# Optimization experiments

Hardware: AMD Instinct MI355X
Metric: run time of the kernel (lower is better)

## Reference

```python
import jax, jax.numpy as jnp
import numpy as np

B, T, I, H = 32, 1024, 512, 512


def _uniform(key, shape, stdv):
    return jax.random.uniform(key, shape, jnp.float32, -stdv, stdv)


def setup_inputs() -> dict:
    key = jax.random.key(0)
    ks = jax.random.split(key, 13)
    stdv = 1.0 / np.sqrt(H)
    return {
        "z": jax.random.normal(ks[0], (B, T, I, 2), jnp.float32),
        "W_zi": _uniform(ks[1], (I, H, 2), stdv), "W_hi": _uniform(ks[2], (H, H, 2), stdv), "b_i": _uniform(ks[3], (H,), stdv),
        "W_zf": _uniform(ks[4], (I, H, 2), stdv), "W_hf": _uniform(ks[5], (H, H, 2), stdv), "b_f": _uniform(ks[6], (H,), stdv),
        "W_zc": _uniform(ks[7], (I, H, 2), stdv), "W_hc": _uniform(ks[8], (H, H, 2), stdv), "b_c": _uniform(ks[9], (H, 2), stdv),
        "W_zo": _uniform(ks[10], (I, H, 2), stdv), "W_ho": _uniform(ks[11], (H, H, 2), stdv), "b_o": _uniform(ks[12], (H,), stdv),
    }


def complex_tanh(zr, zi):
    mag = jnp.maximum(jnp.sqrt(zr * zr + zi * zi + 1e-14), 1e-8)
    t = jnp.tanh(mag)
    return t * (zr / mag), t * (zi / mag)


def reference(z, W_zi, W_hi, b_i, W_zf, W_hf, b_f, W_zc, W_hc, b_c, W_zo, W_ho, b_o):
    zr, zi = z[..., 0], z[..., 1]  # (B,T,I)

    def in_proj_real(Wz):  # real part of complex matmul z @ Wz
        return jnp.einsum('bti,ih->bth', zr, Wz[..., 0]) - jnp.einsum('bti,ih->bth', zi, Wz[..., 1])

    xi = in_proj_real(W_zi)
    xf = in_proj_real(W_zf)
    xo = in_proj_real(W_zo)
    xcr = in_proj_real(W_zc)
    xci = jnp.einsum('bti,ih->bth', zi, W_zc[..., 0]) + jnp.einsum('bti,ih->bth', zr, W_zc[..., 1])

    # time-major for scan: (T,B,H)
    xs = tuple(jnp.swapaxes(a, 0, 1) for a in (xi, xf, xo, xcr, xci))

    def step(carry, x):
        h_r, h_i, c_r, c_i = carry
        xi_t, xf_t, xo_t, xcr_t, xci_t = x
        i_t = jax.nn.sigmoid(xi_t + h_r @ W_hi[..., 0] - h_i @ W_hi[..., 1] + b_i)
        f_t = jax.nn.sigmoid(xf_t + h_r @ W_hf[..., 0] - h_i @ W_hf[..., 1] + b_f)
        o_t = jax.nn.sigmoid(xo_t + h_r @ W_ho[..., 0] - h_i @ W_ho[..., 1] + b_o)
        cr = xcr_t + h_r @ W_hc[..., 0] - h_i @ W_hc[..., 1] + b_c[..., 0]
        ci = xci_t + h_i @ W_hc[..., 0] + h_r @ W_hc[..., 1] + b_c[..., 1]
        ctr, cti = complex_tanh(cr, ci)
        c_r = f_t * c_r + i_t * ctr
        c_i = f_t * c_i + i_t * cti
        hr, hi = complex_tanh(c_r, c_i)
        h_r = o_t * hr
        h_i = o_t * hi
        return (h_r, h_i, c_r, c_i), jnp.stack((h_r, h_i), axis=-1)

    zero = jnp.zeros((z.shape[0], W_hi.shape[0]), z.dtype)
    (h_r, h_i, c_r, c_i), hs = jax.lax.scan(step, (zero, zero, zero, zero), xs)
    hidden_seq = jnp.swapaxes(hs, 0, 1)  # (B,T,H,2)
    h_t = jnp.stack((h_r, h_i), axis=-1)
    c_t = jnp.stack((c_r, c_i), axis=-1)
    return hidden_seq, (h_t, c_t)
```

## Files before the change

### kernel.cpp

```cpp
#include <hip/hip_runtime.h>


#define B_ 32
#define T_ 1024
#define Hd 512
#define Kd 1024
#define Nd 2560
#define Md 32768
#define HS_ELEMS 33554432ull

typedef __attribute__((ext_vector_type(8))) short bf16x8;
typedef __attribute__((ext_vector_type(4))) float f32x4;

__device__ __forceinline__ unsigned short f_bf(float f) {
  unsigned int x; __builtin_memcpy(&x, &f, 4);
  unsigned int r = (x + 0x7FFFu + ((x >> 16) & 1u)) >> 16;
  return (unsigned short)r;
}
__device__ __forceinline__ float bf_f(unsigned short u) {
  unsigned int i = ((unsigned int)u) << 16; float f; __builtin_memcpy(&f, &i, 4); return f;
}
__device__ __forceinline__ float fsig(float x) { return 1.0f / (1.0f + __expf(-x)); }
__device__ __forceinline__ void ctanh_(float zr, float zi, float& tr, float& ti) {
  float m2 = zr * zr + zi * zi + 1e-14f;
  float mag = __fsqrt_rn(m2);
  float e = __expf(2.0f * mag);
  float th = 1.0f - 2.0f / (e + 1.0f);
  float s = th / mag;
  tr = zr * s; ti = zi * s;
}

__device__ __forceinline__ void gl16(const unsigned short* g, unsigned short* l) {
  __builtin_amdgcn_global_load_lds(
      (const __attribute__((address_space(1))) void*)g,
      (__attribute__((address_space(3))) void*)l, 16, 0, 0);
}

__device__ __forceinline__ unsigned int ald(const unsigned int* p) {
  return __hip_atomic_load(p, __ATOMIC_RELAXED, __HIP_MEMORY_SCOPE_AGENT);
}
__device__ __forceinline__ void ast(unsigned int* p, unsigned int v) {
  __hip_atomic_store(p, v, __ATOMIC_RELAXED, __HIP_MEMORY_SCOPE_AGENT);
}

__global__ void build_weights(const float* Wzi, const float* Whi, const float* bi,
                              const float* Wzf, const float* Whf, const float* bfv,
                              const float* Wzc, const float* Whc, const float* bc,
                              const float* Wzo, const float* Who, const float* bo,
                              unsigned short* WzT, unsigned short* WhT, float* bcomb) {
  int n = blockIdx.x;
  int slab = n / 80, wi = n % 80, g = wi / 16, hh = slab * 16 + (wi & 15);
  const float *Wz, *Wh;
  if (g == 0)      { Wz = Wzi; Wh = Whi; }
  else if (g == 1) { Wz = Wzf; Wh = Whf; }
  else if (g == 2) { Wz = Wzo; Wh = Who; }
  else             { Wz = Wzc; Wh = Whc; }
  int q0, q1; float s0, s1;
  if (g < 4) { q0 = 0; s0 = 1.f; q1 = 1; s1 = -1.f; }
  else       { q0 = 1; s0 = 1.f; q1 = 0; s1 =  1.f; }
  for (int k = threadIdx.x; k < Kd; k += 256) {
    int j = k >> 1, p = k & 1;
    int q = p ? q1 : q0; float sg = p ? s1 : s0;
    WzT[(size_t)n * Kd + k] = f_bf(sg * Wz[(j * Hd + hh) * 2 + q]);
    WhT[(size_t)n * Kd + k] = f_bf(sg * Wh[(j * Hd + hh) * 2 + q]);
  }
  if (threadIdx.x == 0) {
    float bv;
    if (g == 0) bv = bi[hh]; else if (g == 1) bv = bfv[hh];
    else if (g == 2) bv = bo[hh];
    else if (g == 3) bv = bc[2 * hh]; else bv = bc[2 * hh + 1];
    bcomb[n] = bv;
  }
}

__global__ void cvt_z(const float4* __restrict__ z, ushort4* __restrict__ Z2) {
  for (size_t i = (size_t)blockIdx.x * 256 + threadIdx.x; i < 8388608ull; i += 8192ull * 256) {
    float4 v = z[i];
    ushort4 o;
    o.x = f_bf(v.x); o.y = f_bf(v.y); o.z = f_bf(v.z); o.w = f_bf(v.w);
    Z2[i] = o;
  }
}

__global__ __launch_bounds__(256) void gemm_x(const unsigned short* __restrict__ Z2,
                                              const unsigned short* __restrict__ WT,
                                              unsigned short* __restrict__ X) {
  __shared__ unsigned short As[128 * 64];
  __shared__ unsigned short Bs[128 * 64];
  int tid = threadIdx.x, lane = tid & 63, wv = tid >> 6;
  int bid = blockIdx.x;
  int mb = bid / (Nd / 128), nb = bid % (Nd / 128);
  size_t m0 = (size_t)mb * 128, n0 = (size_t)nb * 128;
  int wr = wv >> 1, wc = wv & 1;
  int l15 = lane & 15, kg = lane >> 4;
  int lrow = tid >> 3;
  int lcol = (tid & 7) * 8;
  f32x4 acc[4][4] = {};
  for (int k0 = 0; k0 < Kd; k0 += 64) {
    __syncthreads();
#pragma unroll
    for (int c = 0; c < 4; ++c) {
      gl16(Z2 + (m0 + c * 32 + lrow) * Kd + k0 + lcol,
           As + (size_t)c * 2048 + wv * 512);
      gl16(WT + (n0 + c * 32 + lrow) * Kd + k0 + lcol,
           Bs + (size_t)c * 2048 + wv * 512);
    }
    __syncthreads();
#pragma unroll
    for (int ks = 0; ks < 2; ++ks) {
      int kk = ks * 32 + kg * 8;
      bf16x8 a[4], b[4];
#pragma unroll
      for (int i = 0; i < 4; ++i)
        a[i] = *reinterpret_cast<const bf16x8*>(&As[(wr * 64 + i * 16 + l15) * 64 + kk]);
#pragma unroll
      for (int j = 0; j < 4; ++j)
        b[j] = *reinterpret_cast<const bf16x8*>(&Bs[(wc * 64 + j * 16 + l15) * 64 + kk]);
#pragma unroll
      for (int i = 0; i < 4; ++i)
#pragma unroll
        for (int j = 0; j < 4; ++j)
          acc[i][j] = __builtin_amdgcn_mfma_f32_16x16x32_bf16(a[i], b[j], acc[i][j], 0, 0, 0);
    }
  }
#pragma unroll
  for (int i = 0; i < 4; ++i)
#pragma unroll
    for (int j = 0; j < 4; ++j) {
      size_t gm = m0 + wr * 64 + i * 16 + kg * 4;
      size_t gn = n0 + wc * 64 + j * 16 + l15;
#pragma unroll
      for (int r = 0; r < 4; ++r)
        X[(gm + r) * Nd + gn] = f_bf(acc[i][j][r]);
    }
}

#define CHUNK 8
#define STEPB (Nd * 2)
__global__ __launch_bounds__(512) void lstm_all(
    const unsigned short* __restrict__ WhT, const unsigned short* __restrict__ X,
    const float* __restrict__ bcomb, unsigned short* __restrict__ hb,
    int* __restrict__ ctl, float* __restrict__ out) {
  __shared__ unsigned short Xs[2][CHUNK * STEPB / 2];
  __shared__ float xch[8][5][256];
  const int s = blockIdx.x;
  const int tid = threadIdx.x;
  const int wv = tid >> 6, lane = tid & 63;
  const int kh = wv >> 1, mh = wv & 1;
  const int l15 = lane & 15, kg = lane >> 4;
  const int cb = tid >> 4;
  const int ch = tid & 15;
  const int hh = s * 16 + ch;

  unsigned int* flags2 = (unsigned int*)(ctl + 16);
  unsigned int* hbu = (unsigned int*)hb;
  const int pidx = ((s >> 3) * 2 + (wv >> 2)) * 32 + (s & 7) * 4 + (wv & 3);
  const int fbase = (kh * 2 + mh) * 32;
  const int i32 = lane & 31;

  auto stage = [&](int tbase, int buf) {
#pragma unroll
    for (int j = 0; j < 5; ++j) {
      unsigned int P = (unsigned int)(wv * 5 + j) * 1024u + (unsigned int)lane * 16u;
      unsigned int st = P / STEPB, r = P % STEPB;
      unsigned int b = r / 160u, rem = r % 160u;
      gl16(X + ((size_t)b * T_ + (tbase + st)) * Nd + s * 80 + rem / 2,
           &Xs[buf][(size_t)(wv * 5 + j) * 512]);
    }
  };
  stage(0, 0);

  bf16x8 w[5][8];
#pragma unroll
  for (int g = 0; g < 5; ++g)
#pragma unroll
    for (int ks = 0; ks < 8; ++ks)
      w[g][ks] = *reinterpret_cast<const bf16x8*>(
          &WhT[(size_t)(s * 80 + g * 16 + l15) * Kd + kh * 256 + ks * 32 + kg * 8]);

  float bias[5];
#pragma unroll
  for (int g = 0; g < 5; ++g) bias[g] = bcomb[s * 80 + g * 16 + ch];
  float cr = 0.f, ci = 0.f;

  ast(hbu + (size_t)cb * 512 + hh, 0u);
  asm volatile("s_waitcnt vmcnt(0)" ::: "memory");
  if (lane == 0) ast(&flags2[pidx], 1u);

  const int mb = cb >> 4;
  const int xidx = ((cb & 15) >> 2) * 64 + ch * 4 + (cb & 3);

  float2 hist[8];

  for (int tb = 0; tb < T_; tb += 8) {
#pragma unroll
    for (int j = 0; j < 8; ++j) {
      const int t = tb + j;
      const unsigned int need = (unsigned int)(t + 1);
      while (true) {
        unsigned int v = ald(&flags2[fbase + i32]);
        if (__all(v >= need)) break;
      }
      asm volatile("" ::: "memory");

      const unsigned short* hin = hb + (size_t)(t % 3) * 32768;
      unsigned long long hpa = (unsigned long long)(
          hin + (size_t)(mh * 16 + l15) * Kd + kh * 256 + kg * 8);
      bf16x8 a[8];
#define HL(i, off) asm volatile("global_load_dwordx4 %0, %1, off offset:" #off " sc0 sc1" \
                                 : "=v"(a[i]) : "v"(hpa) : "memory")
      HL(0, 0); HL(1, 64); HL(2, 128); HL(3, 192);
      HL(4, 256); HL(5, 320); HL(6, 384); HL(7, 448);
#undef HL
      asm volatile("s_waitcnt vmcnt(0)" ::: "memory");
      __builtin_amdgcn_sched_barrier(0);

      f32x4 acc[5] = {};
#pragma unroll
      for (int ks = 0; ks < 8; ++ks)
#pragma unroll
        for (int g = 0; g < 5; ++g)
          acc[g] = __builtin_amdgcn_mfma_f32_16x16x32_bf16(a[ks], w[g][ks], acc[g], 0, 0, 0);

#pragma unroll
      for (int g = 0; g < 5; ++g)
        *reinterpret_cast<f32x4*>(&xch[wv][g][lane * 4]) = acc[g];
      __syncthreads();

      const unsigned short* xsl = &Xs[(t >> 3) & 1][(t & 7) * Nd + cb * 80 + ch];
      float pre[5];
#pragma unroll
      for (int g = 0; g < 5; ++g) {
        float p = bias[g] + bf_f(xsl[g * 16]);
#pragma unroll
        for (int q = 0; q < 4; ++q) p += xch[q * 2 + mb][g][xidx];
        pre[g] = p;
      }
      float ig = fsig(pre[0]), fg = fsig(pre[1]), og = fsig(pre[2]);
      float ctr, cti; ctanh_(pre[3], pre[4], ctr, cti);
      cr = fg * cr + ig * ctr;
      ci = fg * ci + ig * cti;
      float hr0, hi0; ctanh_(cr, ci, hr0, hi0);
      float hr = og * hr0, hi = og * hi0;
      hist[j] = make_float2(hr, hi);

      unsigned int hv = (unsigned int)f_bf(hr) | ((unsigned int)f_bf(hi) << 16);
      ast(hbu + (size_t)((t + 1) % 3) * 16384 + (size_t)cb * 512 + hh, hv);
      if (t < T_ - 1) {
        asm volatile("s_waitcnt vmcnt(0)" ::: "memory");
        if (lane == 0) ast(&flags2[pidx], (unsigned int)(t + 2));
      }

      if (j == 7) {
#pragma unroll
        for (int q = 0; q < 8; ++q) {
          size_t oidx = ((size_t)cb * T_ + (t - 7 + q)) * (Hd * 2) + hh * 2;
          *reinterpret_cast<float2*>(&out[oidx]) = hist[q];
        }
      }
      if (j == 0 && t + 8 < T_) stage(t + 8, ((t >> 3) + 1) & 1);
      if (t == T_ - 1) {
        size_t fb = HS_ELEMS + ((size_t)cb * Hd + hh) * 2;
        *reinterpret_cast<float2*>(&out[fb]) = make_float2(hr, hi);
        *reinterpret_cast<float2*>(&out[fb + 32768ull]) = make_float2(cr, ci);
      }
      __syncthreads();
    }
  }
}

extern "C" void kernel_launch(void* const* d_in, const int* in_sizes, int n_in,
                              void* d_out, int out_size, void* d_ws, size_t ws_size,
                              hipStream_t stream) {
  const float* z   = (const float*)d_in[0];
  const float* Wzi = (const float*)d_in[1];
  const float* Whi = (const float*)d_in[2];
  const float* bi  = (const float*)d_in[3];
  const float* Wzf = (const float*)d_in[4];
  const float* Whf = (const float*)d_in[5];
  const float* bfv = (const float*)d_in[6];
  const float* Wzc = (const float*)d_in[7];
  const float* Whc = (const float*)d_in[8];
  const float* bc  = (const float*)d_in[9];
  const float* Wzo = (const float*)d_in[10];
  const float* Who = (const float*)d_in[11];
  const float* bo  = (const float*)d_in[12];
  float* out = (float*)d_out;

  size_t off = 0;
  char* ws = (char*)d_ws;
  auto take = [&](size_t nbytes) {
    void* p = ws + off; off += (nbytes + 255) & ~(size_t)255; return p;
  };
  unsigned short* WzT  = (unsigned short*)take((size_t)Nd * Kd * 2);
  unsigned short* WhT  = (unsigned short*)take((size_t)Nd * Kd * 2);
  float*          bcmb = (float*)take(Nd * 4);
  unsigned short* Z2   = (unsigned short*)take((size_t)Md * Kd * 2);
  unsigned short* X    = (unsigned short*)take((size_t)Md * Nd * 2);
  unsigned short* hb   = (unsigned short*)take(3 * 32768 * 2);
  int*            ctl  = (int*)take(4096);

  hipMemsetAsync(ctl, 0, 4096, stream);
  build_weights<<<Nd, 256, 0, stream>>>(Wzi, Whi, bi, Wzf, Whf, bfv,
                                        Wzc, Whc, bc, Wzo, Who, bo,
                                        WzT, WhT, bcmb);
  cvt_z<<<8192, 256, 0, stream>>>((const float4*)z, (ushort4*)Z2);
  gemm_x<<<(Md / 128) * (Nd / 128), 256, 0, stream>>>(Z2, WzT, X);
  lstm_all<<<32, 512, 0, stream>>>(WhT, X, bcmb, hb, ctl, out);
}
```

Baseline: 5.792 ms.

## Switch recurrent step handshake to per-block flags and skip first hidden load

Cross-block synchronisation in the persistent LSTM kernel is simplified. Each wave previously published its own progress flag and polled 32 of them. Now each block publishes a single flag after a block-wide barrier, and each wave polls only the 8 producer-block flags it depends on. The step-0 hidden-state load and the initial zeroing of the hidden buffer are replaced by zero registers, and next-chunk X staging moves to the end of each chunk. The gain is fewer flag reads and writes, at the cost of an extra __syncthreads on the critical path each step and less lead time for the X prefetch.

```diff
diff --git a/kernel.cpp b/kernel.cpp
--- a/kernel.cpp
+++ b/kernel.cpp
@@ -140,7 +140,7 @@
 __global__ __launch_bounds__(512) void lstm_all(
     const unsigned short* __restrict__ WhT, const unsigned short* __restrict__ X,
     const float* __restrict__ bcomb, unsigned short* __restrict__ hb,
-    int* __restrict__ ctl, float* __restrict__ out) {
+    int* __restrict__ flags, float* __restrict__ out) {
   __shared__ unsigned short Xs[2][CHUNK * STEPB / 2];
   __shared__ float xch[8][5][256];
   const int s = blockIdx.x;
@@ -152,12 +152,6 @@
   const int ch = tid & 15;
   const int hh = s * 16 + ch;
 
-  unsigned int* flags2 = (unsigned int*)(ctl + 16);
-  unsigned int* hbu = (unsigned int*)hb;
-  const int pidx = ((s >> 3) * 2 + (wv >> 2)) * 32 + (s & 7) * 4 + (wv & 3);
-  const int fbase = (kh * 2 + mh) * 32;
-  const int i32 = lane & 31;
-
   auto stage = [&](int tbase, int buf) {
 #pragma unroll
     for (int j = 0; j < 5; ++j) {
@@ -183,10 +177,7 @@
   for (int g = 0; g < 5; ++g) bias[g] = bcomb[s * 80 + g * 16 + ch];
   float cr = 0.f, ci = 0.f;
 
-  ast(hbu + (size_t)cb * 512 + hh, 0u);
-  asm volatile("s_waitcnt vmcnt(0)" ::: "memory");
-  if (lane == 0) ast(&flags2[pidx], 1u);
-
+  const int fidx = kh * 8 + (lane & 7);
   const int mb = cb >> 4;
   const int xidx = ((cb & 15) >> 2) * 64 + ch * 4 + (cb & 3);
 
@@ -196,24 +187,31 @@
 #pragma unroll
     for (int j = 0; j < 8; ++j) {
       const int t = tb + j;
-      const unsigned int need = (unsigned int)(t + 1);
-      while (true) {
-        unsigned int v = ald(&flags2[fbase + i32]);
-        if (__all(v >= need)) break;
-      }
-      asm volatile("" ::: "memory");
-
-      const unsigned short* hin = hb + (size_t)(t % 3) * 32768;
-      unsigned long long hpa = (unsigned long long)(
-          hin + (size_t)(mh * 16 + l15) * Kd + kh * 256 + kg * 8);
       bf16x8 a[8];
+      if (t > 0) {
+        const unsigned int need = (unsigned int)(t + 1);
+        while (true) {
+          unsigned int v = ald((const unsigned int*)&flags[fidx]);
+          if (__all(v >= need)) break;
+        }
+        asm volatile("" ::: "memory");
+
+        const unsigned short* hin = hb + (size_t)(t % 3) * 32768;
+        unsigned long long hpa = (unsigned long long)(
+            hin + (size_t)(mh * 16 + l15) * Kd + kh * 256 + kg * 8);
 #define HL(i, off) asm volatile("global_load_dwordx4 %0, %1, off offset:" #off " sc0 sc1" \
-                                 : "=v"(a[i]) : "v"(hpa) : "memory")
-      HL(0, 0); HL(1, 64); HL(2, 128); HL(3, 192);
-      HL(4, 256); HL(5, 320); HL(6, 384); HL(7, 448);
+                                 : "=&v"(a[i]) : "v"(hpa) : "memory")
+        HL(0, 0); HL(1, 64); HL(2, 128); HL(3, 192);
+        HL(4, 256); HL(5, 320); HL(6, 384); HL(7, 448);
 #undef HL
-      asm volatile("s_waitcnt vmcnt(0)" ::: "memory");
-      __builtin_amdgcn_sched_barrier(0);
+        asm volatile("s_waitcnt vmcnt(0)" ::: "memory");
+        __builtin_amdgcn_sched_barrier(0);
+      } else {
+#pragma unroll
+        for (int ks = 0; ks < 8; ++ks)
+#pragma unroll
+          for (int e = 0; e < 8; ++e) a[ks][e] = 0;
+      }
 
       f32x4 acc[5] = {};
 #pragma unroll
@@ -245,10 +243,11 @@
       hist[j] = make_float2(hr, hi);
 
       unsigned int hv = (unsigned int)f_bf(hr) | ((unsigned int)f_bf(hi) << 16);
-      ast(hbu + (size_t)((t + 1) % 3) * 16384 + (size_t)cb * 512 + hh, hv);
+      ast((unsigned int*)hb + (size_t)((t + 1) % 3) * 16384 + (size_t)cb * 512 + hh, hv);
       if (t < T_ - 1) {
         asm volatile("s_waitcnt vmcnt(0)" ::: "memory");
-        if (lane == 0) ast(&flags2[pidx], (unsigned int)(t + 2));
+        __syncthreads();
+        if (tid == 0) ast((unsigned int*)&flags[s], (unsigned int)(t + 2));
       }
 
       if (j == 7) {
@@ -257,8 +256,8 @@
           size_t oidx = ((size_t)cb * T_ + (t - 7 + q)) * (Hd * 2) + hh * 2;
           *reinterpret_cast<float2*>(&out[oidx]) = hist[q];
         }
-      }
-      if (j == 0 && t + 8 < T_) stage(t + 8, ((t >> 3) + 1) & 1);
+        if (t + 1 < T_) stage(t + 1, ((t + 1) >> 3) & 1);
+      }
       if (t == T_ - 1) {
         size_t fb = HS_ELEMS + ((size_t)cb * Hd + hh) * 2;
         *reinterpret_cast<float2*>(&out[fb]) = make_float2(hr, hi);
@@ -298,13 +297,13 @@
   unsigned short* Z2   = (unsigned short*)take((size_t)Md * Kd * 2);
   unsigned short* X    = (unsigned short*)take((size_t)Md * Nd * 2);
   unsigned short* hb   = (unsigned short*)take(3 * 32768 * 2);
-  int*            ctl  = (int*)take(4096);
-
-  hipMemsetAsync(ctl, 0, 4096, stream);
+  int*            flags = (int*)take(64 * 4);
+
+  hipMemsetAsync(flags, 0, 64 * 4, stream);
   build_weights<<<Nd, 256, 0, stream>>>(Wzi, Whi, bi, Wzf, Whf, bfv,
                                         Wzc, Whc, bc, Wzo, Who, bo,
                                         WzT, WhT, bcmb);
   cvt_z<<<8192, 256, 0, stream>>>((const float4*)z, (ushort4*)Z2);
   gemm_x<<<(Md / 128) * (Nd / 128), 256, 0, stream>>>(Z2, WzT, X);
-  lstm_all<<<32, 512, 0, stream>>>(WhT, X, bcmb, hb, ctl, out);
-}
+  lstm_all<<<32, 512, 0, stream>>>(WhT, X, bcmb, hb, flags, out);
+}
```

Measured after the change: 5.339 ms. 1.08x faster.
